# Optimization experiments

Hardware: AMD Instinct MI355X
Metric: run time of the kernel (lower is better)

Reference implementation:

```python
import jax, jax.numpy as jnp
import numpy as np

N_NODES = 100000
N_EDGES = 1600000
IN_DIM, HID_DIM, OUT_DIM = 128, 64, 128


def setup_inputs() -> dict:
    key = jax.random.key(0)
    k1, k2, k3, k4 = jax.random.split(key, 4)
    x = jax.random.normal(k1, (N_NODES, IN_DIM), dtype=jnp.float32)
    edge_index = jax.random.randint(k2, (2, N_EDGES), 0, N_NODES, dtype=jnp.int32)
    W_conv = jax.random.normal(k3, (IN_DIM, HID_DIM), dtype=jnp.float32) * (1.0 / np.sqrt(IN_DIM))
    b_conv = jnp.zeros((HID_DIM,), dtype=jnp.float32)
    W_lin = jax.random.normal(k4, (HID_DIM, OUT_DIM), dtype=jnp.float32) * (1.0 / np.sqrt(HID_DIM))
    b_lin = jnp.zeros((OUT_DIM,), dtype=jnp.float32)
    return {"x": x, "edge_index": edge_index, "W_conv": W_conv, "b_conv": b_conv,
            "W_lin": W_lin, "b_lin": b_lin}


def gcn_conv(x, edge_index, W, b):
    """PyG GCNConv: linear transform, symmetric-normalized aggregation with self-loops, bias."""
    n = x.shape[0]
    loop = jnp.arange(n, dtype=edge_index.dtype)
    src = jnp.concatenate([edge_index[0], loop])  # message sources (x_j)
    dst = jnp.concatenate([edge_index[1], loop])  # aggregation targets
    # degree of target nodes (counting self-loops), D^{-1/2}
    deg = jax.ops.segment_sum(jnp.ones_like(dst, dtype=x.dtype), dst, num_segments=n)
    dinv = jnp.where(deg > 0, jax.lax.rsqrt(deg), 0.0)
    norm = dinv[src] * dinv[dst]  # [E+N]
    h = x @ W  # [N, hid]
    msg = h[src] * norm[:, None]  # gather + normalize, [E+N, hid]
    agg = jax.ops.segment_sum(msg, dst, num_segments=n)  # scatter-add
    return agg + b


def reference(x, edge_index, W_conv, b_conv, W_lin, b_lin):
    h = gcn_conv(x, edge_index, W_conv, b_conv)
    h = jax.nn.relu(h)
    return h @ W_lin + b_lin
```

## Files before the change

kernel.cpp:

```cpp
#include <hip/hip_runtime.h>
#include <hip/hip_bf16.h>

#define NN 100000
#define NE 1600000
#define NBUK 782
#define NBLK 400
#define CHUNK 4000
#define NGB 1563
#define MAXD 64

typedef unsigned short ushort_t;
typedef __bf16 bf16x8 __attribute__((ext_vector_type(8)));
typedef float  f32x4  __attribute__((ext_vector_type(4)));

static __device__ __forceinline__ float bf2f(unsigned u) {
    union { unsigned i; float f; } c; c.i = u << 16; return c.f;
}
static __device__ __forceinline__ float bf2f_hi(unsigned u) {
    union { unsigned i; float f; } c; c.i = u & 0xffff0000u; return c.f;
}
static __device__ __forceinline__ ushort_t f2bf(float f) {
    union { __hip_bfloat16 b; ushort_t u; } c; c.b = __float2bfloat16(f); return c.u;
}

__global__ __launch_bounds__(256) void k_pre(const int* __restrict__ ei,
                                             const float* __restrict__ Wc,
                                             const float* __restrict__ Wl,
                                             int* __restrict__ bhist,
                                             ushort_t* __restrict__ wtb,
                                             ushort_t* __restrict__ w2tb) {
    int b = blockIdx.x, t = threadIdx.x;
    if (b >= NBLK) {
        int i = (b - NBLK) * 256 + t;
        int d = i & 63, k = i >> 6;
        wtb[d * 128 + k] = f2bf(Wc[i]);
        int j = i & 127, k2 = i >> 7;
        w2tb[j * 64 + k2] = f2bf(Wl[i]);
        return;
    }
    __shared__ int h[NBUK];
    for (int i = t; i < NBUK; i += 256) h[i] = 0;
    __syncthreads();
    const int* dst = ei + NE;
    int e0 = b * CHUNK;
    for (int r = t; r < CHUNK; r += 256) atomicAdd(&h[dst[e0 + r] >> 7], 1);
    __syncthreads();
    for (int i = t; i < NBUK; i += 256) bhist[b * NBUK + i] = h[i];
}

__global__ __launch_bounds__(512) void k_colscan(const int* __restrict__ bhist,
                                                 int* __restrict__ basex,
                                                 int* __restrict__ coltot) {
    __shared__ int s[512];
    int k = blockIdx.x, t = threadIdx.x;
    int v = (t < NBLK) ? bhist[t * NBUK + k] : 0;
    s[t] = v;
    __syncthreads();
#pragma unroll
    for (int o = 1; o < 512; o <<= 1) {
        int x = (t >= o) ? s[t - o] : 0;
        __syncthreads();
        s[t] += x;
        __syncthreads();
    }
    if (t < NBLK) basex[t * NBUK + k] = s[t] - v;
    if (t == 511) coltot[k] = s[511];
}

__global__ __launch_bounds__(256) void k_scatter2(const int* __restrict__ ei,
                                                  const int* __restrict__ coltot,
                                                  const int* __restrict__ basex,
                                                  unsigned* __restrict__ ebuf) {
    __shared__ int cur[NBUK];
    __shared__ int bst[NBUK];
    __shared__ int ssum[256];
    int t = threadIdx.x, b = blockIdx.x;
    int v0 = 0, v1 = 0, v2 = 0, v3 = 0;
    int i4 = t * 4;
    if (i4 + 0 < NBUK) v0 = coltot[i4 + 0];
    if (i4 + 1 < NBUK) v1 = coltot[i4 + 1];
    if (i4 + 2 < NBUK) v2 = coltot[i4 + 2];
    if (i4 + 3 < NBUK) v3 = coltot[i4 + 3];
    int tot = v0 + v1 + v2 + v3;
    ssum[t] = tot;
    for (int i = t; i < NBUK; i += 256) cur[i] = 0;
    __syncthreads();
#pragma unroll
    for (int o = 1; o < 256; o <<= 1) {
        int x = (t >= o) ? ssum[t - o] : 0;
        __syncthreads();
        ssum[t] += x;
        __syncthreads();
    }
    int run = ssum[t] - tot;
    if (i4 + 0 < NBUK) { bst[i4 + 0] = run; run += v0; }
    if (i4 + 1 < NBUK) { bst[i4 + 1] = run; run += v1; }
    if (i4 + 2 < NBUK) { bst[i4 + 2] = run; run += v2; }
    if (i4 + 3 < NBUK) { bst[i4 + 3] = run; run += v3; }
    __syncthreads();

    int e0 = b * CHUNK;
    for (int r = t; r < CHUNK; r += 256) {
        int e = e0 + r;
        int sv = ei[e];
        int dv = ei[NE + e];
        int k = dv >> 7;
        int rk = atomicAdd(&cur[k], 1);
        int pos = bst[k] + basex[b * NBUK + k] + rk;
        ebuf[pos] = (unsigned)sv | ((unsigned)(dv & 127) << 17);
    }
}

__global__ __launch_bounds__(256) void k_sortgemm(const int* __restrict__ coltot,
                                                  const unsigned* __restrict__ ebuf,
                                                  const float* __restrict__ x,
                                                  const ushort_t* __restrict__ wtb,
                                                  int* __restrict__ csrp,
                                                  int* __restrict__ deg,
                                                  float* __restrict__ dinv,
                                                  ushort_t* __restrict__ hp) {
    __shared__ int cur[128];
    __shared__ int ssum[256];
    __shared__ float sdv[128];
    int t = threadIdx.x, b = blockIdx.x;
    int s = 0;
    for (int i = t; i < b; i += 256) s += coltot[i];
    ssum[t] = s;
    if (t < 128) cur[t] = 0;
    __syncthreads();
#pragma unroll
    for (int o = 128; o > 0; o >>= 1) {
        if (t < o) ssum[t] += ssum[t + o];
        __syncthreads();
    }
    int base = ssum[0];
    int ne = coltot[b];
    for (int i = t; i < ne; i += 256) {
        unsigned pe = ebuf[base + i];
        int nl = pe >> 17;
        int rk = atomicAdd(&cur[nl], 1);
        if (rk < MAXD) csrp[(b * 128 + nl) * MAXD + rk] = (int)(pe & 0x1FFFF);
    }
    __syncthreads();
    if (t < 128) {
        int node = b * 128 + t;
        int dg = cur[t];
        float dvv = rsqrtf((float)dg + 1.0f);
        deg[node]  = dg;
        dinv[node] = dvv;
        sdv[t]     = dvv;
    }
    __syncthreads();

    int w = t >> 6, lane = t & 63, l15 = lane & 15, quad = lane >> 4;
#pragma unroll 1
    for (int half = 0; half < 2; ++half) {
        int nl = half * 64 + w * 16 + l15;
        int gn = b * 128 + nl;
        int gnc = gn < NN ? gn : NN - 1;
        const float*    xp = x   + (size_t)gnc * 128 + quad * 8;
        const ushort_t* wp = wtb + l15 * 128 + quad * 8;
        f32x4 acc[4];
#pragma unroll
        for (int dt = 0; dt < 4; ++dt) { acc[dt][0]=0.f; acc[dt][1]=0.f; acc[dt][2]=0.f; acc[dt][3]=0.f; }

#pragma unroll
        for (int kt = 0; kt < 4; ++kt) {
            float4 v0 = *(const float4*)(xp + kt * 32);
            float4 v1 = *(const float4*)(xp + kt * 32 + 4);
            union { ushort_t u[8]; bf16x8 v; } cv;
            cv.u[0]=f2bf(v0.x); cv.u[1]=f2bf(v0.y); cv.u[2]=f2bf(v0.z); cv.u[3]=f2bf(v0.w);
            cv.u[4]=f2bf(v1.x); cv.u[5]=f2bf(v1.y); cv.u[6]=f2bf(v1.z); cv.u[7]=f2bf(v1.w);
            bf16x8 bv = cv.v;
#pragma unroll
            for (int dt = 0; dt < 4; ++dt) {
                bf16x8 av = *(const bf16x8*)(wp + dt * 16 * 128 + kt * 32);
                acc[dt] = __builtin_amdgcn_mfma_f32_16x16x32_bf16(av, bv, acc[dt], 0, 0, 0);
            }
        }
        if (gn < NN) {
            float dv = sdv[nl];
#pragma unroll
            for (int dt = 0; dt < 4; ++dt) {
                uint2 o;
                o.x = (unsigned)f2bf(dv * acc[dt][0]) | ((unsigned)f2bf(dv * acc[dt][1]) << 16);
                o.y = (unsigned)f2bf(dv * acc[dt][2]) | ((unsigned)f2bf(dv * acc[dt][3]) << 16);
                *(uint2*)&hp[(size_t)gn * 64 + dt * 16 + quad * 4] = o;
            }
        }
    }
}

__global__ __launch_bounds__(512, 4) void k_gafin(const int* __restrict__ deg,
                                                  const float* __restrict__ dinv,
                                                  const int* __restrict__ csrp,
                                                  const ushort_t* __restrict__ hp,
                                                  const float* __restrict__ b_conv,
                                                  const ushort_t* __restrict__ w2tb,
                                                  const float* __restrict__ blin,
                                                  float* __restrict__ out) {
    __shared__ __align__(16) ushort_t as[64 * 72];
    int t = threadIdx.x;
    int w = t >> 6, lane = t & 63;
    int g = lane >> 3, l8 = lane & 7;
    int node0 = blockIdx.x * 64;

    int nl = w * 8 + g;
    int node = node0 + nl;
    int nodeR = node < NN ? node : NN - 1;
    int cntt = deg[node];
    int cnt = cntt < MAXD ? cntt : MAXD;
    const ushort_t* hpc = hp + l8 * 8;

    uint4 colvA = make_uint4(0u, 0u, 0u, 0u);
    uint4 colvB = make_uint4(0u, 0u, 0u, 0u);
    if (l8 * 8 < cnt)     colvA = *(const uint4*)(csrp + node * MAXD + l8 * 8);
    if (l8 * 8 + 4 < cnt) colvB = *(const uint4*)(csrp + node * MAXD + l8 * 8 + 4);

    int cmax = cnt;
    { int o1 = __shfl_xor(cmax, 8, 64);  cmax = cmax > o1 ? cmax : o1;
      int o2 = __shfl_xor(cmax, 16, 64); cmax = cmax > o2 ? cmax : o2;
      int o3 = __shfl_xor(cmax, 32, 64); cmax = cmax > o3 ? cmax : o3; }

    float s0 = 0.f, s1 = 0.f, s2 = 0.f, s3 = 0.f;
    float s4 = 0.f, s5 = 0.f, s6 = 0.f, s7 = 0.f;
#pragma unroll 1
    for (int j0 = 0; j0 < cmax; j0 += 8) {
        int sl = (lane & 56) + (j0 >> 3);
        int cc[8];
        cc[0] = __shfl((int)colvA.x, sl, 64);
        cc[1] = __shfl((int)colvA.y, sl, 64);
        cc[2] = __shfl((int)colvA.z, sl, 64);
        cc[3] = __shfl((int)colvA.w, sl, 64);
        cc[4] = __shfl((int)colvB.x, sl, 64);
        cc[5] = __shfl((int)colvB.y, sl, 64);
        cc[6] = __shfl((int)colvB.z, sl, 64);
        cc[7] = __shfl((int)colvB.w, sl, 64);
        int jrem = cnt - j0;
        uint4 dd[8];
#pragma unroll
        for (int u = 0; u < 8; ++u) {
            int c = (u < jrem) ? cc[u] : nodeR;
            dd[u] = *(const uint4*)(hpc + (size_t)c * 64);
        }
#pragma unroll
        for (int u = 0; u < 8; ++u) {
            if (u >= jrem) { dd[u].x = 0u; dd[u].y = 0u; dd[u].z = 0u; dd[u].w = 0u; }
            s0 += bf2f(dd[u].x); s1 += bf2f_hi(dd[u].x);
            s2 += bf2f(dd[u].y); s3 += bf2f_hi(dd[u].y);
            s4 += bf2f(dd[u].z); s5 += bf2f_hi(dd[u].z);
            s6 += bf2f(dd[u].w); s7 += bf2f_hi(dd[u].w);
        }
    }
    uint4 sl4 = *(const uint4*)(hpc + (size_t)nodeR * 64);
    s0 += bf2f(sl4.x); s1 += bf2f_hi(sl4.x);
    s2 += bf2f(sl4.y); s3 += bf2f_hi(sl4.y);
    s4 += bf2f(sl4.z); s5 += bf2f_hi(sl4.z);
    s6 += bf2f(sl4.w); s7 += bf2f_hi(sl4.w);
    float dv = dinv[node];
    float4 bc0 = *(const float4*)(b_conv + l8 * 8);
    float4 bc1 = *(const float4*)(b_conv + l8 * 8 + 4);
    float v0 = fmaxf(dv * s0 + bc0.x, 0.f);
    float v1 = fmaxf(dv * s1 + bc0.y, 0.f);
    float v2 = fmaxf(dv * s2 + bc0.z, 0.f);
    float v3 = fmaxf(dv * s3 + bc0.w, 0.f);
    float v4 = fmaxf(dv * s4 + bc1.x, 0.f);
    float v5 = fmaxf(dv * s5 + bc1.y, 0.f);
    float v6 = fmaxf(dv * s6 + bc1.z, 0.f);
    float v7 = fmaxf(dv * s7 + bc1.w, 0.f);
    uint4 o;
    o.x = (unsigned)f2bf(v0) | ((unsigned)f2bf(v1) << 16);
    o.y = (unsigned)f2bf(v2) | ((unsigned)f2bf(v3) << 16);
    o.z = (unsigned)f2bf(v4) | ((unsigned)f2bf(v5) << 16);
    o.w = (unsigned)f2bf(v6) | ((unsigned)f2bf(v7) << 16);
    *(uint4*)&as[nl * 72 + l8 * 8] = o;
    __syncthreads();

    int l15 = lane & 15, quad = lane >> 4;
    int nb0 = (w & 3) * 16, jh = (w >> 2) * 64;
    int gn = node0 + nb0 + l15;
    const ushort_t* ap = &as[(nb0 + l15) * 72 + quad * 8];
    const ushort_t* wp = w2tb + (jh + l15) * 64 + quad * 8;
    f32x4 acc[4];
#pragma unroll
    for (int jt = 0; jt < 4; ++jt) { acc[jt][0]=0.f; acc[jt][1]=0.f; acc[jt][2]=0.f; acc[jt][3]=0.f; }

#pragma unroll
    for (int kt = 0; kt < 2; ++kt) {
        bf16x8 bv = *(const bf16x8*)(ap + kt * 32);
#pragma unroll
        for (int jt = 0; jt < 4; ++jt) {
            bf16x8 av = *(const bf16x8*)(wp + jt * 16 * 64 + kt * 32);
            acc[jt] = __builtin_amdgcn_mfma_f32_16x16x32_bf16(av, bv, acc[jt], 0, 0, 0);
        }
    }
    if (gn < NN) {
#pragma unroll
        for (int jt = 0; jt < 4; ++jt) {
            int j0 = jh + jt * 16 + quad * 4;
            float4 b4 = *(const float4*)(blin + j0);
            float4 o2;
            o2.x = acc[jt][0] + b4.x; o2.y = acc[jt][1] + b4.y;
            o2.z = acc[jt][2] + b4.z; o2.w = acc[jt][3] + b4.w;
            *(float4*)&out[(size_t)gn * 128 + j0] = o2;
        }
    }
}

extern "C" void kernel_launch(void* const* d_in, const int* in_sizes, int n_in,
                              void* d_out, int out_size, void* d_ws, size_t ws_size,
                              hipStream_t stream) {
    const float* x  = (const float*)d_in[0];
    const int*   ei = (const int*)d_in[1];
    const float* Wc = (const float*)d_in[2];
    const float* bc = (const float*)d_in[3];
    const float* Wl = (const float*)d_in[4];
    const float* bl = (const float*)d_in[5];
    float* out = (float*)d_out;

    char* ws = (char*)d_ws;
    int*      bhist  = (int*)(ws + 0);
    int*      basex  = (int*)(ws + 1251200);
    int*      coltot = (int*)(ws + 2502400);
    int*      deg    = (int*)(ws + 2512064);
    float*    dinv   = (float*)(ws + 2912448);
    ushort_t* wtb    = (ushort_t*)(ws + 3312832);
    ushort_t* w2tb   = (ushort_t*)(ws + 3329216);
    unsigned* ebuf   = (unsigned*)(ws + 3345600);
    int*      csrp   = (int*)(ws + 9745600);
    ushort_t* hp     = (ushort_t*)(ws + 35370176);

    k_pre     <<<NBLK + 32, 256, 0, stream>>>(ei, Wc, Wl, bhist, wtb, w2tb);
    k_colscan <<<NBUK, 512, 0, stream>>>(bhist, basex, coltot);
    k_scatter2<<<NBLK, 256, 0, stream>>>(ei, coltot, basex, ebuf);
    k_sortgemm<<<NBUK, 256, 0, stream>>>(coltot, ebuf, x, wtb, csrp, deg, dinv, hp);
    k_gafin   <<<NGB, 512, 0, stream>>>(deg, dinv, csrp, hp, bc, w2tb, bl, out);
}
```

Baseline: 235.6 us.

## Split bf16 hidden features into two 32-wide halves gathered in separate passes

The projected hidden matrix is now stored as two separate 32-column planes instead of one 64-column row per node. The aggregation kernel gathers neighbours in two passes, each reading 64-byte rows (8-byte loads per lane) from one plane. This shrinks the working set of each pass so it can stay in L2/MALL cache better during the random gathers. In exchange, the neighbour index shuffles and loop overhead run twice, and each gathered row is smaller.

```diff
diff --git a/kernel.cpp b/kernel.cpp
--- a/kernel.cpp
+++ b/kernel.cpp
@@ -8,6 +8,7 @@
 #define CHUNK 4000
 #define NGB 1563
 #define MAXD 64
+#define HS ((size_t)100096 * 32)
 
 typedef unsigned short ushort_t;
 typedef __bf16 bf16x8 __attribute__((ext_vector_type(8)));
@@ -185,7 +186,7 @@
                 uint2 o;
                 o.x = (unsigned)f2bf(dv * acc[dt][0]) | ((unsigned)f2bf(dv * acc[dt][1]) << 16);
                 o.y = (unsigned)f2bf(dv * acc[dt][2]) | ((unsigned)f2bf(dv * acc[dt][3]) << 16);
-                *(uint2*)&hp[(size_t)gn * 64 + dt * 16 + quad * 4] = o;
+                *(uint2*)&hp[(size_t)(dt >> 1) * HS + (size_t)gn * 32 + (dt & 1) * 16 + quad * 4] = o;
             }
         }
     }
@@ -210,7 +211,6 @@
     int nodeR = node < NN ? node : NN - 1;
     int cntt = deg[node];
     int cnt = cntt < MAXD ? cntt : MAXD;
-    const ushort_t* hpc = hp + l8 * 8;
 
     uint4 colvA = make_uint4(0u, 0u, 0u, 0u);
     uint4 colvB = make_uint4(0u, 0u, 0u, 0u);
@@ -222,58 +222,51 @@
       int o2 = __shfl_xor(cmax, 16, 64); cmax = cmax > o2 ? cmax : o2;
       int o3 = __shfl_xor(cmax, 32, 64); cmax = cmax > o3 ? cmax : o3; }
 
-    float s0 = 0.f, s1 = 0.f, s2 = 0.f, s3 = 0.f;
-    float s4 = 0.f, s5 = 0.f, s6 = 0.f, s7 = 0.f;
+    float dv = dinv[node];
+
 #pragma unroll 1
-    for (int j0 = 0; j0 < cmax; j0 += 8) {
-        int sl = (lane & 56) + (j0 >> 3);
-        int cc[8];
-        cc[0] = __shfl((int)colvA.x, sl, 64);
-        cc[1] = __shfl((int)colvA.y, sl, 64);
-        cc[2] = __shfl((int)colvA.z, sl, 64);
-        cc[3] = __shfl((int)colvA.w, sl, 64);
-        cc[4] = __shfl((int)colvB.x, sl, 64);
-        cc[5] = __shfl((int)colvB.y, sl, 64);
-        cc[6] = __shfl((int)colvB.z, sl, 64);
-        cc[7] = __shfl((int)colvB.w, sl, 64);
-        int jrem = cnt - j0;
-        uint4 dd[8];
-#pragma unroll
-        for (int u = 0; u < 8; ++u) {
-            int c = (u < jrem) ? cc[u] : nodeR;
-            dd[u] = *(const uint4*)(hpc + (size_t)c * 64);
-        }
-#pragma unroll
-        for (int u = 0; u < 8; ++u) {
-            if (u >= jrem) { dd[u].x = 0u; dd[u].y = 0u; dd[u].z = 0u; dd[u].w = 0u; }
-            s0 += bf2f(dd[u].x); s1 += bf2f_hi(dd[u].x);
-            s2 += bf2f(dd[u].y); s3 += bf2f_hi(dd[u].y);
-            s4 += bf2f(dd[u].z); s5 += bf2f_hi(dd[u].z);
-            s6 += bf2f(dd[u].w); s7 += bf2f_hi(dd[u].w);
-        }
-    }
-    uint4 sl4 = *(const uint4*)(hpc + (size_t)nodeR * 64);
-    s0 += bf2f(sl4.x); s1 += bf2f_hi(sl4.x);
-    s2 += bf2f(sl4.y); s3 += bf2f_hi(sl4.y);
-    s4 += bf2f(sl4.z); s5 += bf2f_hi(sl4.z);
-    s6 += bf2f(sl4.w); s7 += bf2f_hi(sl4.w);
-    float dv = dinv[node];
-    float4 bc0 = *(const float4*)(b_conv + l8 * 8);
-    float4 bc1 = *(const float4*)(b_conv + l8 * 8 + 4);
-    float v0 = fmaxf(dv * s0 + bc0.x, 0.f);
-    float v1 = fmaxf(dv * s1 + bc0.y, 0.f);
-    float v2 = fmaxf(dv * s2 + bc0.z, 0.f);
-    float v3 = fmaxf(dv * s3 + bc0.w, 0.f);
-    float v4 = fmaxf(dv * s4 + bc1.x, 0.f);
-    float v5 = fmaxf(dv * s5 + bc1.y, 0.f);
-    float v6 = fmaxf(dv * s6 + bc1.z, 0.f);
-    float v7 = fmaxf(dv * s7 + bc1.w, 0.f);
-    uint4 o;
-    o.x = (unsigned)f2bf(v0) | ((unsigned)f2bf(v1) << 16);
-    o.y = (unsigned)f2bf(v2) | ((unsigned)f2bf(v3) << 16);
-    o.z = (unsigned)f2bf(v4) | ((unsigned)f2bf(v5) << 16);
-    o.w = (unsigned)f2bf(v6) | ((unsigned)f2bf(v7) << 16);
-    *(uint4*)&as[nl * 72 + l8 * 8] = o;
+    for (int h = 0; h < 2; ++h) {
+        const ushort_t* hpc = hp + (size_t)h * HS + l8 * 4;
+        float s0 = 0.f, s1 = 0.f, s2 = 0.f, s3 = 0.f;
+#pragma unroll 1
+        for (int j0 = 0; j0 < cmax; j0 += 8) {
+            int sl = (lane & 56) + (j0 >> 3);
+            int cc[8];
+            cc[0] = __shfl((int)colvA.x, sl, 64);
+            cc[1] = __shfl((int)colvA.y, sl, 64);
+            cc[2] = __shfl((int)colvA.z, sl, 64);
+            cc[3] = __shfl((int)colvA.w, sl, 64);
+            cc[4] = __shfl((int)colvB.x, sl, 64);
+            cc[5] = __shfl((int)colvB.y, sl, 64);
+            cc[6] = __shfl((int)colvB.z, sl, 64);
+            cc[7] = __shfl((int)colvB.w, sl, 64);
+            int jrem = cnt - j0;
+            uint2 dd[8];
+#pragma unroll
+            for (int u = 0; u < 8; ++u) {
+                int c = (u < jrem) ? cc[u] : nodeR;
+                dd[u] = *(const uint2*)(hpc + (size_t)c * 32);
+            }
+#pragma unroll
+            for (int u = 0; u < 8; ++u) {
+                if (u >= jrem) { dd[u].x = 0u; dd[u].y = 0u; }
+                s0 += bf2f(dd[u].x); s1 += bf2f_hi(dd[u].x);
+                s2 += bf2f(dd[u].y); s3 += bf2f_hi(dd[u].y);
+            }
+        }
+        uint2 sl2 = *(const uint2*)(hpc + (size_t)nodeR * 32);
+        s0 += bf2f(sl2.x); s1 += bf2f_hi(sl2.x);
+        s2 += bf2f(sl2.y); s3 += bf2f_hi(sl2.y);
+        float4 bch = *(const float4*)(b_conv + h * 32 + l8 * 4);
+        float v0 = fmaxf(dv * s0 + bch.x, 0.f);
+        float v1 = fmaxf(dv * s1 + bch.y, 0.f);
+        float v2 = fmaxf(dv * s2 + bch.z, 0.f);
+        float v3 = fmaxf(dv * s3 + bch.w, 0.f);
+        uint2 o;
+        o.x = (unsigned)f2bf(v0) | ((unsigned)f2bf(v1) << 16);
+        o.y = (unsigned)f2bf(v2) | ((unsigned)f2bf(v3) << 16);
+        *(uint2*)&as[nl * 72 + h * 32 + l8 * 4] = o;
+    }
     __syncthreads();
 
     int l15 = lane & 15, quad = lane >> 4;
```

After: 234.4 us. About the same (-0.5%).
